# Optimization experiments

Hardware: AMD Instinct MI355X
Metric: run time of the kernel (lower is better)

## Reference

```python
import jax, jax.numpy as jnp
import numpy as np

B, L, K, E, H, NH, W_OFF = 8, 512, 16, 32, 1, 64, 1
DK = E // H


def setup_inputs() -> dict:
    key = jax.random.key(0)
    ks = jax.random.split(key, 12)
    return {
        "time_steps": jax.random.uniform(ks[0], (B, L), jnp.float32),
        "val": jax.random.normal(ks[1], (B, L), jnp.float32),
        "mark": jax.random.randint(ks[2], (B, L), 1, K + 1, dtype=jnp.int32),
        "non_pad_mask": jnp.ones((B, L, 1), jnp.float32),
        "Wl": jax.random.normal(ks[3], (1, 1), jnp.float32) * 0.5,
        "bl": jnp.zeros((1,), jnp.float32),
        "Wp": jax.random.normal(ks[4], (E - 1, 1), jnp.float32) * 0.5,
        "bp": jnp.zeros((E - 1,), jnp.float32),
        "Wq": jax.random.normal(ks[5], (E, E), jnp.float32) / np.sqrt(E).astype(np.float32),
        "bq": jnp.zeros((E,), jnp.float32),
        "Wk": jax.random.normal(ks[6], (E, E), jnp.float32) / np.sqrt(E).astype(np.float32),
        "bk": jnp.zeros((E,), jnp.float32),
        "Wo": jax.random.normal(ks[7], (NH, K * H), jnp.float32) / np.sqrt(K * H).astype(np.float32),
        "bo": jnp.zeros((NH,), jnp.float32),
        "W_ih": jax.random.normal(ks[8], (3 * NH, NH), jnp.float32) / np.sqrt(NH).astype(np.float32),
        "W_hh": jax.random.normal(ks[9], (3 * NH, NH), jnp.float32) / np.sqrt(NH).astype(np.float32),
        "b_ih": jnp.zeros((3 * NH,), jnp.float32),
        "b_hh": jnp.zeros((3 * NH,), jnp.float32),
    }


def _forward(time_steps, val, mark, non_pad_mask,
             Wl, bl, Wp, bp, Wq, bq, Wk, bk, Wo, bo,
             W_ih, W_hh, b_ih, b_hh):
    # transform_to_3d_ts: scatter each (b,l) event into its channel mark-1
    npm = non_pad_mask[:, :, 0]                       # [B,L]
    onehot = (mark - 1)[:, :, None] == jnp.arange(K)[None, None, :]  # [B,L,K]
    valid = onehot & (npm > 0)[:, :, None]
    val_blk = jnp.where(valid, val[:, :, None], 0.0)          # [B,L,K]
    mask_blk = jnp.where(valid, npm[:, :, None], 0.0)         # [B,L,K]

    # learn_time_embedding
    tt = time_steps[:, :, None]                                # [B,L,1]
    key_emb = jnp.concatenate([tt @ Wl.T + bl, jnp.sin(tt @ Wp.T + bp)], axis=-1)  # [B,L,E]

    # subsequent mask (tril with diag offset w)
    att_mask = jnp.tril(jnp.ones((L, L), jnp.float32), W_OFF)  # [L,L]

    # multiTimeAttention (query == key == key_emb)
    q = (key_emb @ Wq.T + bq).reshape(B, L, H, DK).transpose(0, 2, 1, 3)  # [B,H,L,DK]
    k = (key_emb @ Wk.T + bk).reshape(B, L, H, DK).transpose(0, 2, 1, 3)
    scores = jnp.einsum('bhqd,bhkd->bhqk', q, k) / jnp.sqrt(jnp.float32(DK))  # [B,H,L,L]
    # broadcast to [B,H,L,L,K] (repeat_interleave equivalent), apply att_mask then pad mask
    scores5 = scores[..., None] * att_mask[None, None, :, :, None]
    scores5 = jnp.where(mask_blk[:, None, None, :, :] == 0, -1e9, scores5)
    p_attn = jax.nn.softmax(scores5, axis=-2)                  # softmax over key positions
    x = jnp.sum(p_attn * val_blk[:, None, None, :, :], axis=-2)  # [B,H,L,K]
    x = x.transpose(0, 2, 1, 3).reshape(B, L, H * K)
    att_out = x @ Wo.T + bo                                    # [B,L,NH]

    # single-layer GRU over time (PyTorch gate equations)
    def step(h, xt):
        gi = xt @ W_ih.T + b_ih
        gh = h @ W_hh.T + b_hh
        ir, iz, inn = jnp.split(gi, 3, axis=-1)
        hr, hz, hn = jnp.split(gh, 3, axis=-1)
        r = jax.nn.sigmoid(ir + hr)
        z = jax.nn.sigmoid(iz + hz)
        n = jnp.tanh(inn + r * hn)
        h_new = (1.0 - z) * n + z * h
        return h_new, h_new

    h0 = jnp.zeros((B, NH), att_out.dtype)
    _, outs = jax.lax.scan(step, h0, att_out.transpose(1, 0, 2))  # [L,B,NH]
    return outs.transpose(1, 0, 2)                                # [B,L,NH]


def reference(time_steps, val, mark, non_pad_mask,
              Wl, bl, Wp, bp, Wq, bq, Wk, bk, Wo, bo,
              W_ih, W_hh, b_ih, b_hh):
    return _forward(time_steps, val, mark, non_pad_mask,
                    Wl, bl, Wp, bp, Wq, bq, Wk, bk, Wo, bo,
                    W_ih, W_hh, b_ih, b_hh)
```

## Files before the change

kernel.cpp:

```cpp
#include <hip/hip_runtime.h>
#include <math.h>

#define B_    8
#define L_    512
#define K_    16
#define E_    32
#define NH_   64
#define WOFF_ 1


typedef float v2f __attribute__((ext_vector_type(2)));
typedef float v4f __attribute__((ext_vector_type(4)));

__global__ __launch_bounds__(256) void k_embed(
    const float* __restrict__ ts, const float* __restrict__ Wl,
    const float* __restrict__ bl, const float* __restrict__ Wp,
    const float* __restrict__ bp, const float* __restrict__ Wq,
    const float* __restrict__ bq, const float* __restrict__ Wk,
    const float* __restrict__ bk,
    float* __restrict__ qmat, float* __restrict__ kmatT)
{
    __shared__ float WqL[1024], WkL[1024];
    __shared__ float bqL[32], bkL[32], WpL[31], bpL[31];
    __shared__ float wl0, bl0;
    const int tid = threadIdx.x;

    {
        float4 v = ((const float4*)Wq)[tid];
        ((float4*)WqL)[tid] = v;
        float4 u = ((const float4*)Wk)[tid];
        ((float4*)WkL)[tid] = u;
    }
    if (tid < 32) { bqL[tid] = bq[tid]; bkL[tid] = bk[tid]; }
    if (tid < 31) { WpL[tid] = Wp[tid]; bpL[tid] = bp[tid]; }
    if (tid == 0) { wl0 = Wl[0]; bl0 = bl[0]; }
    __syncthreads();

    const int p = blockIdx.x * 256 + tid;
    const float t = ts[p];
    float e[32];
    e[0] = t * wl0 + bl0;
    #pragma unroll
    for (int j = 1; j < 32; ++j) e[j] = sinf(t * WpL[j - 1] + bpL[j - 1]);

    const int b = p >> 9, l = p & 511;
    float4* qm4 = (float4*)(qmat + (size_t)p * 32);
    float*  kT  = kmatT + (size_t)b * 32 * 512 + l;

    for (int dq = 0; dq < 8; ++dq) {
        float q0 = bqL[4*dq+0], q1 = bqL[4*dq+1], q2 = bqL[4*dq+2], q3 = bqL[4*dq+3];
        float k0 = bkL[4*dq+0], k1 = bkL[4*dq+1], k2 = bkL[4*dq+2], k3 = bkL[4*dq+3];
        const float* wq = &WqL[(4*dq) * 32];
        const float* wk = &WkL[(4*dq) * 32];
        #pragma unroll
        for (int j = 0; j < 32; ++j) {
            const float ej = e[j];
            q0 = fmaf(wq[j],      ej, q0);
            q1 = fmaf(wq[32 + j], ej, q1);
            q2 = fmaf(wq[64 + j], ej, q2);
            q3 = fmaf(wq[96 + j], ej, q3);
            k0 = fmaf(wk[j],      ej, k0);
            k1 = fmaf(wk[32 + j], ej, k1);
            k2 = fmaf(wk[64 + j], ej, k2);
            k3 = fmaf(wk[96 + j], ej, k3);
        }
        qm4[dq] = make_float4(q0, q1, q2, q3);
        kT[(4*dq + 0) * 512] = k0;
        kT[(4*dq + 1) * 512] = k1;
        kT[(4*dq + 2) * 512] = k2;
        kT[(4*dq + 3) * 512] = k3;
    }
}

__global__ __launch_bounds__(256) void k_attn_gi(
    const float* __restrict__ qmat, const float* __restrict__ kmatT,
    const float* __restrict__ val,  const int*   __restrict__ mark,
    const float* __restrict__ npm,  const float* __restrict__ Wo,
    const float* __restrict__ bo,   const float* __restrict__ Wih,
    const float* __restrict__ bih,  float* __restrict__ gi)
{
    __shared__ float srow[4 * 512];
    __shared__ int   cc[512];
    __shared__ float vv[512];
    __shared__ float WL[192 * 65];
    __shared__ float bL[192];
    __shared__ float attL[16 * 64];
    const int tid = threadIdx.x;
    const int qb  = blockIdx.x;
    const int b   = blockIdx.y;

    for (int k = tid; k < 512; k += 256) {
        const int   m  = mark[b * 512 + k];
        const float np = npm[b * 512 + k];
        cc[k] = (np > 0.0f) ? (m - 1) : -1;
        vv[k] = val[b * 512 + k];
    }
    for (int idx = tid; idx < 3072; idx += 256) {
        float4 v = ((const float4*)Wih)[idx];
        const int g = idx >> 4, jq = idx & 15;
        float* dst = &WL[g * 65 + jq * 4];
        dst[0] = v.x; dst[1] = v.y; dst[2] = v.z; dst[3] = v.w;
    }
    if (tid < 192) bL[tid] = bih[tid];
    __syncthreads();

    const int w = tid >> 6, lane = tid & 63;
    const float* kTb = kmatT + (size_t)b * 32 * 512;

    for (int iq = 0; iq < 4; ++iq) {
        const int q = qb * 16 + w * 4 + iq;

        float qr[32];
        const float4* qm4 = (const float4*)(qmat + (size_t)(b * 512 + q) * 32);
        #pragma unroll
        for (int j4 = 0; j4 < 8; ++j4) {
            float4 v = qm4[j4];
            qr[4*j4+0] = v.x; qr[4*j4+1] = v.y; qr[4*j4+2] = v.z; qr[4*j4+3] = v.w;
        }

        float acc[8];
        #pragma unroll
        for (int m = 0; m < 8; ++m) acc[m] = 0.0f;
        #pragma unroll 4
        for (int j = 0; j < 32; ++j) {
            const float* row = kTb + j * 512 + lane;
            const float  qj  = qr[j];
            #pragma unroll
            for (int m = 0; m < 8; ++m) acc[m] = fmaf(qj, row[m * 64], acc[m]);
        }
        #pragma unroll
        for (int m = 0; m < 8; ++m)
            srow[w * 512 + m * 64 + lane] = acc[m] * 0.17677669529663687f;
        __syncthreads();

        const int c = lane & 15, s = lane >> 4;
        float mx = -1e30f, Z = 0.0f, X = 0.0f;
        const int base = s * 128;
        for (int t = 0; t < 128; ++t) {
            const int k = base + ((t + s) & 127);
            if (cc[k] == c) {
                const float l  = (k <= q + WOFF_) ? srow[w * 512 + k] : 0.0f;
                const float mn = fmaxf(mx, l);
                const float e1 = __expf(l - mn);
                const float sc = __expf(mx - mn);
                Z = Z * sc + e1;
                X = X * sc + e1 * vv[k];
                mx = mn;
            }
        }
        #pragma unroll
        for (int off = 16; off <= 32; off <<= 1) {
            const float mo = __shfl_xor(mx, off);
            const float Zo = __shfl_xor(Z, off);
            const float Xo = __shfl_xor(X, off);
            const float mn = fmaxf(mx, mo);
            const float a0 = __expf(mx - mn);
            const float a1 = __expf(mo - mn);
            Z = Z * a0 + Zo * a1;
            X = X * a0 + Xo * a1;
            mx = mn;
        }
        const float x = (Z > 0.0f) ? X / Z : 0.0f;

        float xs[16];
        #pragma unroll
        for (int c2 = 0; c2 < 16; ++c2) xs[c2] = __shfl(x, c2);

        const float4* wo4 = (const float4*)(Wo + lane * 16);
        float a = bo[lane];
        #pragma unroll
        for (int c4 = 0; c4 < 4; ++c4) {
            float4 v = wo4[c4];
            a += xs[4*c4+0] * v.x + xs[4*c4+1] * v.y + xs[4*c4+2] * v.z + xs[4*c4+3] * v.w;
        }
        attL[(w * 4 + iq) * 64 + lane] = a;
        __syncthreads();
    }

    const size_t out0 = (size_t)(b * 32 + qb) * 16 * 192;
    for (int pp = 0; pp < 12; ++pp) {
        const int p = tid + 256 * pp;
        const int r = p / 192, g = p - r * 192;
        float a0 = bL[g], a1 = 0.f, a2 = 0.f, a3 = 0.f;
        const float* wrow = &WL[g * 65];
        const float* arow = &attL[r * 64];
        #pragma unroll
        for (int j = 0; j < 64; j += 4) {
            a0 = fmaf(arow[j + 0], wrow[j + 0], a0);
            a1 = fmaf(arow[j + 1], wrow[j + 1], a1);
            a2 = fmaf(arow[j + 2], wrow[j + 2], a2);
            a3 = fmaf(arow[j + 3], wrow[j + 3], a3);
        }
        gi[out0 + p] = (a0 + a1) + (a2 + a3);
    }
}


#define GRU_STEP(u, DO_REFILL) {                                           \
    v4f hv[16];                                                            \
                                       \
    _Pragma("unroll")                                                      \
    for (int k = 0; k < 6; ++k) hv[k] = hs4[k];                            \
    const float gr = pr[u], gz = pz[u], gn = pn[u];                        \
    if (DO_REFILL) {                                                       \
        pr[u] = pf[0];                                                     \
        pz[u] = pf[64];                                                    \
        pn[u] = pf[128];                                                   \
        pf += 192;                                                         \
    }                                                                      \
    v2f ar2 = {gr + br, 0.0f};                                             \
    v2f az2 = {gz + bz, 0.0f};                                             \
    v2f an2 = {bn, 0.0f};                                                  \
    _Pragma("unroll")                                                      \
    for (int k = 0; k < 16; ++k) {                                         \
        if (k < 10) hv[k + 6] = hs4[k + 6];              \
        v2f p0 = __builtin_shufflevector(hv[k], hv[k], 0, 1);              \
        v2f p1 = __builtin_shufflevector(hv[k], hv[k], 2, 3);              \
        ar2 = wr[2*k]     * p0 + ar2;                    \
        az2 = wz[2*k]     * p0 + az2;                                      \
        an2 = wn[2*k]     * p0 + an2;                                      \
        ar2 = wr[2*k + 1] * p1 + ar2;                                      \
        az2 = wz[2*k + 1] * p1 + az2;                                      \
        an2 = wn[2*k + 1] * p1 + an2;                                      \
    }                                                                      \
    const float ar = ar2.x + ar2.y;                                        \
    const float az = az2.x + az2.y;                                        \
    const float hn = an2.x + an2.y;                                        \
    const float r = __builtin_amdgcn_rcpf(1.0f + __expf(-ar));             \
    const float z = __builtin_amdgcn_rcpf(1.0f + __expf(-az));             \
    float npre = gn + r * hn;                                              \
    npre = fminf(fmaxf(npre, -15.0f), 15.0f);                              \
    const float e2 = __expf(2.0f * npre);                                  \
    const float n  = (e2 - 1.0f) * __builtin_amdgcn_rcpf(e2 + 1.0f);       \
    h = fmaf(z, h - n, n);                              \
    hs[lane] = h;                        \
    *outp = h;                                        \
    outp += 64;                                                            \
}

__global__ __launch_bounds__(64, 1) void k_gru(
    const float* __restrict__ gi, const float* __restrict__ Whh,
    const float* __restrict__ bhh, float* __restrict__ out)
{
    __shared__ float hs[64];
    const int lane = threadIdx.x;
    const int b    = blockIdx.x;

    v2f wr[32], wz[32], wn[32];
    {
        const v2f* r2 = (const v2f*)(Whh + (size_t)lane * 64);
        const v2f* z2 = (const v2f*)(Whh + (size_t)(lane + 64) * 64);
        const v2f* n2 = (const v2f*)(Whh + (size_t)(lane + 128) * 64);
        #pragma unroll
        for (int j = 0; j < 32; ++j) {
            wr[j] = r2[j];
            wz[j] = z2[j];
            wn[j] = n2[j];
        }
    }
    const float br = bhh[lane];
    const float bz = bhh[lane + 64];
    const float bn = bhh[lane + 128];

    const float* gib  = gi  + (size_t)b * 512 * 192;
    float*       outp = out + (size_t)b * 512 * 64 + lane;

    float h = 0.0f;
    hs[lane] = 0.0f;

    float pr[2], pz[2], pn[2];
    #pragma unroll
    for (int i = 0; i < 2; ++i) {
        const float* gp = gib + (size_t)i * 192;
        pr[i] = gp[lane];
        pz[i] = gp[lane + 64];
        pn[i] = gp[lane + 128];
    }
    const float* pf = gib + (size_t)2 * 192 + lane;

    const v4f* hs4 = (const v4f*)hs;

    for (int tt = 0; tt < 510; tt += 2) {
        GRU_STEP(0, 1)
        GRU_STEP(1, 1)
    }
    GRU_STEP(0, 0)
    GRU_STEP(1, 0)
}

extern "C" void kernel_launch(void* const* d_in, const int* in_sizes, int n_in,
                              void* d_out, int out_size, void* d_ws, size_t ws_size,
                              hipStream_t stream)
{
    const float* ts   = (const float*)d_in[0];
    const float* val  = (const float*)d_in[1];
    const int*   mark = (const int*)  d_in[2];
    const float* npm  = (const float*)d_in[3];
    const float* Wl   = (const float*)d_in[4];
    const float* bl   = (const float*)d_in[5];
    const float* Wp   = (const float*)d_in[6];
    const float* bp   = (const float*)d_in[7];
    const float* Wq   = (const float*)d_in[8];
    const float* bq   = (const float*)d_in[9];
    const float* Wk   = (const float*)d_in[10];
    const float* bk   = (const float*)d_in[11];
    const float* Wo   = (const float*)d_in[12];
    const float* bo   = (const float*)d_in[13];
    const float* Wih  = (const float*)d_in[14];
    const float* Whh  = (const float*)d_in[15];
    const float* bih  = (const float*)d_in[16];
    const float* bhh  = (const float*)d_in[17];

    float* ws    = (float*)d_ws;
    float* qmat  = ws;
    float* kmatT = ws + 131072;
    float* gi    = ws + 524288;
    float* out   = (float*)d_out;

    k_embed<<<16, 256, 0, stream>>>(ts, Wl, bl, Wp, bp, Wq, bq, Wk, bk, qmat, kmatT);
    k_attn_gi<<<dim3(32, 8), 256, 0, stream>>>(qmat, kmatT, val, mark, npm, Wo, bo, Wih, bih, gi);
    k_gru<<<8, 64, 0, stream>>>(gi, Whh, bhh, out);
}
```

Measured before the change: 380.1 us.

## Fuse time embedding and Q/K projection into attention kernel, recompute K per block

Merges the embedding/projection kernel into the attention+input-gate kernel. Each block recomputes all 512 keys for its batch into shared memory and computes only its own 16 queries, which removes the global qmat/kmatT round trip and one launch. To free LDS for the 64KB key tile, W_ih and b_ih are now read directly from global memory instead of being staged in shared memory. The cost is 32x redundant sin and key-projection work per batch, plus higher LDS use that may lower occupancy.

New measurement: 384.5 us. No clear change (+1.1%).

```diff
diff --git a/kernel.cpp b/kernel.cpp
--- a/kernel.cpp
+++ b/kernel.cpp
@@ -12,18 +12,31 @@
 typedef float v2f __attribute__((ext_vector_type(2)));
 typedef float v4f __attribute__((ext_vector_type(4)));
 
-__global__ __launch_bounds__(256) void k_embed(
-    const float* __restrict__ ts, const float* __restrict__ Wl,
-    const float* __restrict__ bl, const float* __restrict__ Wp,
-    const float* __restrict__ bp, const float* __restrict__ Wq,
-    const float* __restrict__ bq, const float* __restrict__ Wk,
-    const float* __restrict__ bk,
-    float* __restrict__ qmat, float* __restrict__ kmatT)
+__global__ __launch_bounds__(256) void k_fused(
+    const float* __restrict__ ts,   const float* __restrict__ val,
+    const int*   __restrict__ mark, const float* __restrict__ npm,
+    const float* __restrict__ Wl,   const float* __restrict__ bl,
+    const float* __restrict__ Wp,   const float* __restrict__ bp,
+    const float* __restrict__ Wq,   const float* __restrict__ bq,
+    const float* __restrict__ Wk,   const float* __restrict__ bk,
+    const float* __restrict__ Wo,   const float* __restrict__ bo,
+    const float* __restrict__ Wih,  const float* __restrict__ bih,
+    float* __restrict__ gi)
 {
+    __shared__ float kL[32 * 512];
+    __shared__ float qL[16 * 32];
+    __shared__ float srow[4 * 512];
+    __shared__ int   cc[512];
+    __shared__ float vv[512];
+    __shared__ float attL[16 * 64];
     __shared__ float WqL[1024], WkL[1024];
     __shared__ float bqL[32], bkL[32], WpL[31], bpL[31];
     __shared__ float wl0, bl0;
+
     const int tid = threadIdx.x;
+    const int qb  = blockIdx.x;
+    const int b   = blockIdx.y;
+    const int qb0 = qb * 16;
 
     {
         float4 v = ((const float4*)Wq)[tid];
@@ -34,84 +47,67 @@
     if (tid < 32) { bqL[tid] = bq[tid]; bkL[tid] = bk[tid]; }
     if (tid < 31) { WpL[tid] = Wp[tid]; bpL[tid] = bp[tid]; }
     if (tid == 0) { wl0 = Wl[0]; bl0 = bl[0]; }
-    __syncthreads();
-
-    const int p = blockIdx.x * 256 + tid;
-    const float t = ts[p];
-    float e[32];
-    e[0] = t * wl0 + bl0;
-    #pragma unroll
-    for (int j = 1; j < 32; ++j) e[j] = sinf(t * WpL[j - 1] + bpL[j - 1]);
-
-    const int b = p >> 9, l = p & 511;
-    float4* qm4 = (float4*)(qmat + (size_t)p * 32);
-    float*  kT  = kmatT + (size_t)b * 32 * 512 + l;
-
-    for (int dq = 0; dq < 8; ++dq) {
-        float q0 = bqL[4*dq+0], q1 = bqL[4*dq+1], q2 = bqL[4*dq+2], q3 = bqL[4*dq+3];
-        float k0 = bkL[4*dq+0], k1 = bkL[4*dq+1], k2 = bkL[4*dq+2], k3 = bkL[4*dq+3];
-        const float* wq = &WqL[(4*dq) * 32];
-        const float* wk = &WkL[(4*dq) * 32];
-        #pragma unroll
-        for (int j = 0; j < 32; ++j) {
-            const float ej = e[j];
-            q0 = fmaf(wq[j],      ej, q0);
-            q1 = fmaf(wq[32 + j], ej, q1);
-            q2 = fmaf(wq[64 + j], ej, q2);
-            q3 = fmaf(wq[96 + j], ej, q3);
-            k0 = fmaf(wk[j],      ej, k0);
-            k1 = fmaf(wk[32 + j], ej, k1);
-            k2 = fmaf(wk[64 + j], ej, k2);
-            k3 = fmaf(wk[96 + j], ej, k3);
-        }
-        qm4[dq] = make_float4(q0, q1, q2, q3);
-        kT[(4*dq + 0) * 512] = k0;
-        kT[(4*dq + 1) * 512] = k1;
-        kT[(4*dq + 2) * 512] = k2;
-        kT[(4*dq + 3) * 512] = k3;
-    }
-}
-
-__global__ __launch_bounds__(256) void k_attn_gi(
-    const float* __restrict__ qmat, const float* __restrict__ kmatT,
-    const float* __restrict__ val,  const int*   __restrict__ mark,
-    const float* __restrict__ npm,  const float* __restrict__ Wo,
-    const float* __restrict__ bo,   const float* __restrict__ Wih,
-    const float* __restrict__ bih,  float* __restrict__ gi)
-{
-    __shared__ float srow[4 * 512];
-    __shared__ int   cc[512];
-    __shared__ float vv[512];
-    __shared__ float WL[192 * 65];
-    __shared__ float bL[192];
-    __shared__ float attL[16 * 64];
-    const int tid = threadIdx.x;
-    const int qb  = blockIdx.x;
-    const int b   = blockIdx.y;
-
     for (int k = tid; k < 512; k += 256) {
         const int   m  = mark[b * 512 + k];
         const float np = npm[b * 512 + k];
         cc[k] = (np > 0.0f) ? (m - 1) : -1;
         vv[k] = val[b * 512 + k];
     }
-    for (int idx = tid; idx < 3072; idx += 256) {
-        float4 v = ((const float4*)Wih)[idx];
-        const int g = idx >> 4, jq = idx & 15;
-        float* dst = &WL[g * 65 + jq * 4];
-        dst[0] = v.x; dst[1] = v.y; dst[2] = v.z; dst[3] = v.w;
-    }
-    if (tid < 192) bL[tid] = bih[tid];
     __syncthreads();
 
+    for (int l = tid; l < 512; l += 256) {
+        const float t = ts[b * 512 + l];
+        float e[32];
+        e[0] = t * wl0 + bl0;
+        #pragma unroll
+        for (int j = 1; j < 32; ++j) e[j] = sinf(t * WpL[j - 1] + bpL[j - 1]);
+
+        const bool ownq = (l >= qb0) && (l < qb0 + 16);
+        float* qrow = qL + (l - qb0) * 32;
+
+        for (int dq = 0; dq < 8; ++dq) {
+            float k0 = bkL[4*dq+0], k1 = bkL[4*dq+1], k2 = bkL[4*dq+2], k3 = bkL[4*dq+3];
+            const float* wk = &WkL[(4*dq) * 32];
+            #pragma unroll
+            for (int j = 0; j < 32; ++j) {
+                const float ej = e[j];
+                k0 = fmaf(wk[j],      ej, k0);
+                k1 = fmaf(wk[32 + j], ej, k1);
+                k2 = fmaf(wk[64 + j], ej, k2);
+                k3 = fmaf(wk[96 + j], ej, k3);
+            }
+            kL[(4*dq + 0) * 512 + l] = k0;
+            kL[(4*dq + 1) * 512 + l] = k1;
+            kL[(4*dq + 2) * 512 + l] = k2;
+            kL[(4*dq + 3) * 512 + l] = k3;
+
+            if (ownq) {
+                float q0 = bqL[4*dq+0], q1 = bqL[4*dq+1], q2 = bqL[4*dq+2], q3 = bqL[4*dq+3];
+                const float* wq = &WqL[(4*dq) * 32];
+                #pragma unroll
+                for (int j = 0; j < 32; ++j) {
+                    const float ej = e[j];
+                    q0 = fmaf(wq[j],      ej, q0);
+                    q1 = fmaf(wq[32 + j], ej, q1);
+                    q2 = fmaf(wq[64 + j], ej, q2);
+                    q3 = fmaf(wq[96 + j], ej, q3);
+                }
+                qrow[4*dq + 0] = q0;
+                qrow[4*dq + 1] = q1;
+                qrow[4*dq + 2] = q2;
+                qrow[4*dq + 3] = q3;
+            }
+        }
+    }
+    __syncthreads();
+
     const int w = tid >> 6, lane = tid & 63;
-    const float* kTb = kmatT + (size_t)b * 32 * 512;
 
     for (int iq = 0; iq < 4; ++iq) {
-        const int q = qb * 16 + w * 4 + iq;
+        const int q = qb0 + w * 4 + iq;
 
         float qr[32];
-        const float4* qm4 = (const float4*)(qmat + (size_t)(b * 512 + q) * 32);
+        const float4* qm4 = (const float4*)(qL + (size_t)(q - qb0) * 32);
         #pragma unroll
         for (int j4 = 0; j4 < 8; ++j4) {
             float4 v = qm4[j4];
@@ -123,7 +119,7 @@
         for (int m = 0; m < 8; ++m) acc[m] = 0.0f;
         #pragma unroll 4
         for (int j = 0; j < 32; ++j) {
-            const float* row = kTb + j * 512 + lane;
+            const float* row = kL + j * 512 + lane;
             const float  qj  = qr[j];
             #pragma unroll
             for (int m = 0; m < 8; ++m) acc[m] = fmaf(qj, row[m * 64], acc[m]);
@@ -181,8 +177,8 @@
     for (int pp = 0; pp < 12; ++pp) {
         const int p = tid + 256 * pp;
         const int r = p / 192, g = p - r * 192;
-        float a0 = bL[g], a1 = 0.f, a2 = 0.f, a3 = 0.f;
-        const float* wrow = &WL[g * 65];
+        float a0 = bih[g], a1 = 0.f, a2 = 0.f, a3 = 0.f;
+        const float* wrow = Wih + g * 64;
         const float* arow = &attL[r * 64];
         #pragma unroll
         for (int j = 0; j < 64; j += 4) {
@@ -312,12 +308,10 @@
     const float* bhh  = (const float*)d_in[17];
 
     float* ws    = (float*)d_ws;
-    float* qmat  = ws;
-    float* kmatT = ws + 131072;
     float* gi    = ws + 524288;
     float* out   = (float*)d_out;
 
-    k_embed<<<16, 256, 0, stream>>>(ts, Wl, bl, Wp, bp, Wq, bq, Wk, bk, qmat, kmatT);
-    k_attn_gi<<<dim3(32, 8), 256, 0, stream>>>(qmat, kmatT, val, mark, npm, Wo, bo, Wih, bih, gi);
+    k_fused<<<dim3(32, 8), 256, 0, stream>>>(ts, val, mark, npm, Wl, bl, Wp, bp,
+                                             Wq, bq, Wk, bk, Wo, bo, Wih, bih, gi);
     k_gru<<<8, 64, 0, stream>>>(gi, Whh, bhh, out);
 }
```
